# Performance work log

Measured on AMD Instinct MI355X. Metric: run time of the kernel, lower is better.

## Reference

```python
import jax, jax.numpy as jnp
import numpy as np

TEMPERATURE = 0.07


def setup_inputs() -> dict:
    key = jax.random.key(0)
    k1, k2 = jax.random.split(key)
    B, D = 8192, 256
    embeddings = jax.random.normal(k1, (B, D), dtype=jnp.float32)
    ids = jax.random.randint(k2, (B,), 0, 1024, dtype=jnp.int64 if jax.config.jax_enable_x64 else jnp.int32)
    return {"embeddings": embeddings, "ids": ids}


def reference(embeddings, ids):
    B = embeddings.shape[0]
    # L2-normalize rows (F.normalize with p=2, dim=1)
    emb = embeddings / jnp.maximum(jnp.linalg.norm(embeddings, axis=1, keepdims=True), 1e-12)
    sim = (emb @ emb.T) / TEMPERATURE                      # [B, B]
    eye = jnp.eye(B, dtype=bool)
    sim = jnp.where(eye, -jnp.inf, sim)
    exp_sim = jnp.exp(sim)                                  # diag -> 0
    pos_mask = (ids[:, None] == ids[None, :]) & ~eye        # [B, B]
    pos_sum = jnp.sum(jnp.where(pos_mask, exp_sim, 0.0), axis=1)  # [B]
    all_sum = jnp.sum(exp_sim, axis=1)                      # [B]
    valid = pos_mask.any(axis=1)
    per_row = -jnp.log(pos_sum / all_sum)
    loss = jnp.sum(jnp.where(valid, per_row, 0.0))
    n_valid = jnp.sum(valid.astype(jnp.float32))
    return loss / jnp.maximum(n_valid, 1.0)
```

## Files before the change

kernel.cpp:

```cpp
#include <hip/hip_runtime.h>
#include <hip/hip_bf16.h>

#define B_SZ 8192
#define D_SZ 256
#define NTILES 2080
#define GRID_SIM 512
#define PRESCALE 4.539816004686735f

typedef __attribute__((ext_vector_type(4))) float f32x4;
typedef __attribute__((ext_vector_type(8))) short s16x8;

__global__ __launch_bounds__(256) void norm_kernel(const float* __restrict__ emb,
                                                   ushort* __restrict__ nbf,
                                                   float* __restrict__ sums) {
    sums[blockIdx.x * 64 + (threadIdx.x >> 2)] = 0.0f;

    const int wave = threadIdx.x >> 6, lane = threadIdx.x & 63;
    for (int g = blockIdx.x; g < B_SZ / 4; g += 256) {
        const int row = g * 4 + wave;
        const float4 v = ((const float4*)(emb + (size_t)row * D_SZ))[lane];
        float ss = v.x * v.x + v.y * v.y + v.z * v.z + v.w * v.w;
        #pragma unroll
        for (int m = 1; m < 64; m <<= 1) ss += __shfl_xor(ss, m, 64);
        float s = PRESCALE / fmaxf(sqrtf(ss), 1e-12f);
        __hip_bfloat16 b0 = __float2bfloat16(v.x * s);
        __hip_bfloat16 b1 = __float2bfloat16(v.y * s);
        __hip_bfloat16 b2 = __float2bfloat16(v.z * s);
        __hip_bfloat16 b3 = __float2bfloat16(v.w * s);
        ushort4 o;
        o.x = *(ushort*)&b0; o.y = *(ushort*)&b1; o.z = *(ushort*)&b2; o.w = *(ushort*)&b3;
        ((ushort4*)(nbf + (size_t)row * D_SZ))[lane] = o;
    }
}

__device__ __forceinline__ void decode_tile(int tb, int& i0, int& j0, bool& diag) {
    int bj = (int)((sqrtf(8.0f * tb + 1.0f) - 1.0f) * 0.5f);
    while ((bj + 1) * (bj + 2) / 2 <= tb) ++bj;
    while (bj * (bj + 1) / 2 > tb) --bj;
    const int bi = tb - bj * (bj + 1) / 2;
    i0 = bi * 128; j0 = bj * 128; diag = (bi == bj);
}

__device__ __forceinline__ void gload16(const ushort* g, ushort* l) {
    __builtin_amdgcn_global_load_lds(
        (const __attribute__((address_space(1))) unsigned int*)g,
        (__attribute__((address_space(3))) unsigned int*)l,
        16, 0, 0);
}

__device__ __forceinline__ void issue_stage(ushort* bA,
                                            const ushort* __restrict__ N,
                                            int i0, int j0, int k0,
                                            int wave, int r, int c8s) {
    ushort* bB = bA + 8192;
    const ushort* gA = N + (size_t)(i0 + wave * 32) * D_SZ + k0;
    const ushort* gB = N + (size_t)(j0 + wave * 32) * D_SZ + k0;
    #pragma unroll
    for (int q = 0; q < 4; ++q) {
        gload16(gA + (size_t)(q * 8 + r) * D_SZ + c8s, bA + (wave * 32 + q * 8) * 64);
        gload16(gB + (size_t)(q * 8 + r) * D_SZ + c8s, bB + (wave * 32 + q * 8) * 64);
    }
}

__global__ __launch_bounds__(256) void sim_kernel(const ushort* __restrict__ N,
                                                  const int* __restrict__ ids,
                                                  float* __restrict__ all_sum,
                                                  float* __restrict__ pos_sum) {
    __shared__ ushort smem[4 * 128 * 64];

    const int t    = threadIdx.x;
    const int wave = t >> 6, lane = t & 63;
    const int wy   = wave >> 1, wx = wave & 1;
    const int r    = lane >> 3;
    const int c8s  = ((lane & 7) ^ r) * 8;
    const int myc  = lane & 15;

    int tb = blockIdx.x;
    int i0, j0; bool diag;
    decode_tile(tb, i0, j0, diag);

    issue_stage(smem, N, i0, j0, 0, wave, r, c8s);

    while (true) {
        const int ntb = tb + GRID_SIM;
        const bool have_next = (ntb < NTILES);
        int ni0 = i0, nj0 = j0; bool ndiag = diag;
        if (have_next) decode_tile(ntb, ni0, nj0, ndiag);

        f32x4 acc[4][4];
        #pragma unroll
        for (int mi = 0; mi < 4; ++mi)
            #pragma unroll
            for (int ni = 0; ni < 4; ++ni)
                acc[mi][ni] = (f32x4){0.f, 0.f, 0.f, 0.f};

        #pragma unroll
        for (int kk = 0; kk < 4; ++kk) {
            ushort* bA = smem + (kk & 1) * 16384;
            ushort* bW = smem + ((kk + 1) & 1) * 16384;
            ushort* bB = bA + 8192;

            asm volatile("s_waitcnt vmcnt(0)" ::: "memory");
            __syncthreads();
            if (kk < 3)           issue_stage(bW, N, i0, j0, (kk + 1) * 64, wave, r, c8s);
            else if (have_next)   issue_stage(bW, N, ni0, nj0, 0, wave, r, c8s);

            #pragma unroll
            for (int ks = 0; ks < 2; ++ks) {
                const int C = ks * 4 + (lane >> 4);
                const int slot = (C ^ (lane & 7)) * 8;
                s16x8 af[4], bf[4];
                #pragma unroll
                for (int mi = 0; mi < 4; ++mi)
                    af[mi] = *(const s16x8*)&bA[(wy * 64 + mi * 16 + (lane & 15)) * 64 + slot];
                #pragma unroll
                for (int ni = 0; ni < 4; ++ni)
                    bf[ni] = *(const s16x8*)&bB[(wx * 64 + ni * 16 + (lane & 15)) * 64 + slot];
                #pragma unroll
                for (int mi = 0; mi < 4; ++mi)
                    #pragma unroll
                    for (int ni = 0; ni < 4; ++ni)
                        acc[mi][ni] = __builtin_amdgcn_mfma_f32_16x16x32_bf16(
                            af[mi], bf[ni], acc[mi][ni], 0, 0, 0);
            }
        }

        __syncthreads();
        float* rowAllPart = (float*)&smem[16384];
        float* rowPosPart = (float*)&smem[24576];

        int idc[4];
        #pragma unroll
        for (int ni = 0; ni < 4; ++ni)
            idc[ni] = ids[j0 + wx * 64 + ni * 16 + myc];

        float cAll[4] = {0.f, 0.f, 0.f, 0.f};
        float cPos[4] = {0.f, 0.f, 0.f, 0.f};

        #pragma unroll
        for (int mi = 0; mi < 4; ++mi) {
            float rAll[4] = {0.f, 0.f, 0.f, 0.f};
            float rPos[4] = {0.f, 0.f, 0.f, 0.f};
            const int rbase = wy * 64 + mi * 16 + (lane >> 4) * 4;
            const int4 idr  = *(const int4*)&ids[i0 + rbase];
            #pragma unroll
            for (int ni = 0; ni < 4; ++ni) {
                const int cloc = wx * 64 + ni * 16 + myc;
                #pragma unroll
                for (int rg = 0; rg < 4; ++rg) {
                    const int lr = rbase + rg;
                    float e = __builtin_amdgcn_exp2f(acc[mi][ni][rg]);
                    if (diag && lr == cloc) e = 0.0f;
                    rAll[rg] += e; cAll[ni] += e;
                    const int idrv = (rg == 0) ? idr.x : (rg == 1) ? idr.y
                                   : (rg == 2) ? idr.z : idr.w;
                    if (idrv == idc[ni]) { rPos[rg] += e; cPos[ni] += e; }
                }
            }
            #pragma unroll
            for (int rg = 0; rg < 4; ++rg) {
                rowAllPart[(rbase + rg) * 32 + wx * 16 + myc] = rAll[rg];
                rowPosPart[(rbase + rg) * 32 + wx * 16 + myc] = rPos[rg];
            }
        }

        if (!diag) {
            #pragma unroll
            for (int ni = 0; ni < 4; ++ni) {
                cAll[ni] += __shfl_xor(cAll[ni], 16, 64);
                cAll[ni] += __shfl_xor(cAll[ni], 32, 64);
                cPos[ni] += __shfl_xor(cPos[ni], 16, 64);
                cPos[ni] += __shfl_xor(cPos[ni], 32, 64);
            }
            if (lane < 16) {
                #pragma unroll
                for (int ni = 0; ni < 4; ++ni) {
                    const int gc = j0 + wx * 64 + ni * 16 + lane;
                    atomicAdd(&all_sum[gc], cAll[ni]);
                    if (cPos[ni] != 0.0f) atomicAdd(&pos_sum[gc], cPos[ni]);
                }
            }
        }

        __syncthreads();
        {
            const int row = t & 127;
            const float* src = (t >= 128) ? rowPosPart : rowAllPart;
            float s = 0.0f;
            #pragma unroll
            for (int k8 = 0; k8 < 8; ++k8) {
                const int chunk = (k8 + (row & 7)) & 7;
                const float4 v = *(const float4*)&src[row * 32 + chunk * 4];
                s += v.x + v.y + v.z + v.w;
            }
            float* dst = (t >= 128) ? pos_sum : all_sum;
            atomicAdd(&dst[i0 + row], s);
        }

        if (!have_next) break;
        tb = ntb; i0 = ni0; j0 = nj0; diag = ndiag;
    }
}

__global__ __launch_bounds__(256) void loss_kernel(const float* __restrict__ all_sum,
                                                   const float* __restrict__ pos_sum,
                                                   float* __restrict__ out) {
    float loss = 0.0f, cnt = 0.0f;
    for (int i = threadIdx.x; i < B_SZ; i += 256) {
        float p = pos_sum[i], a = all_sum[i];
        if (p > 0.0f) { loss += logf(a) - logf(p); cnt += 1.0f; }
    }
    #pragma unroll
    for (int m = 1; m < 64; m <<= 1) {
        loss += __shfl_xor(loss, m, 64);
        cnt  += __shfl_xor(cnt, m, 64);
    }
    __shared__ float sl[4], sc[4];
    int wave = threadIdx.x >> 6, lane = threadIdx.x & 63;
    if (lane == 0) { sl[wave] = loss; sc[wave] = cnt; }
    __syncthreads();
    if (threadIdx.x == 0) {
        float L = sl[0] + sl[1] + sl[2] + sl[3];
        float C = sc[0] + sc[1] + sc[2] + sc[3];
        out[0] = L / fmaxf(C, 1.0f);
    }
}

extern "C" void kernel_launch(void* const* d_in, const int* in_sizes, int n_in,
                              void* d_out, int out_size, void* d_ws, size_t ws_size,
                              hipStream_t stream) {
    const float* emb = (const float*)d_in[0];
    const int*   ids = (const int*)d_in[1];
    float*       out = (float*)d_out;

    float*  all_sum = (float*)d_ws;
    float*  pos_sum = all_sum + B_SZ;
    ushort* nbf     = (ushort*)((char*)d_ws + 65536);

    norm_kernel<<<256, 256, 0, stream>>>(emb, nbf, all_sum);
    sim_kernel<<<GRID_SIM, 256, 0, stream>>>(nbf, ids, all_sum, pos_sum);
    loss_kernel<<<1, 256, 0, stream>>>(all_sum, pos_sum, out);
}
```

Before: 118.2 us.

## Use eight waves per tile and reduce row partials with shuffles

The similarity kernel now runs 512 threads per block (eight waves in a 2x4 grid), so each wave computes a 64x32 sub-tile instead of 64x64. Each wave loads half as many rows per stage, and register use per thread drops. Row partial sums are now reduced within the wave by xor shuffles and written to small dedicated shared arrays. This removes the 32-way shared-memory partial reduction and the extra barrier before the epilogue. More waves per CU should improve latency hiding, at the cost of more shuffle work and more LDS fragment reads per MFMA, since A fragments are reloaded by four waves instead of two.

```diff
diff --git a/kernel.cpp b/kernel.cpp
--- a/kernel.cpp
+++ b/kernel.cpp
@@ -53,27 +53,29 @@
                                             int i0, int j0, int k0,
                                             int wave, int r, int c8s) {
     ushort* bB = bA + 8192;
-    const ushort* gA = N + (size_t)(i0 + wave * 32) * D_SZ + k0;
-    const ushort* gB = N + (size_t)(j0 + wave * 32) * D_SZ + k0;
+    const ushort* gA = N + (size_t)(i0 + wave * 16) * D_SZ + k0;
+    const ushort* gB = N + (size_t)(j0 + wave * 16) * D_SZ + k0;
     #pragma unroll
-    for (int q = 0; q < 4; ++q) {
-        gload16(gA + (size_t)(q * 8 + r) * D_SZ + c8s, bA + (wave * 32 + q * 8) * 64);
-        gload16(gB + (size_t)(q * 8 + r) * D_SZ + c8s, bB + (wave * 32 + q * 8) * 64);
-    }
-}
-
-__global__ __launch_bounds__(256) void sim_kernel(const ushort* __restrict__ N,
-                                                  const int* __restrict__ ids,
-                                                  float* __restrict__ all_sum,
-                                                  float* __restrict__ pos_sum) {
+    for (int q = 0; q < 2; ++q) {
+        gload16(gA + (size_t)(q * 8 + r) * D_SZ + c8s, bA + (wave * 16 + q * 8) * 64);
+        gload16(gB + (size_t)(q * 8 + r) * D_SZ + c8s, bB + (wave * 16 + q * 8) * 64);
+    }
+}
+
+__global__ __launch_bounds__(512, 4) void sim_kernel(const ushort* __restrict__ N,
+                                                     const int* __restrict__ ids,
+                                                     float* __restrict__ all_sum,
+                                                     float* __restrict__ pos_sum) {
     __shared__ ushort smem[4 * 128 * 64];
+    __shared__ float rowAllPart[128 * 4];
+    __shared__ float rowPosPart[128 * 4];
 
     const int t    = threadIdx.x;
     const int wave = t >> 6, lane = t & 63;
-    const int wy   = wave >> 1, wx = wave & 1;
+    const int wy   = wave >> 2, wx = wave & 3;
     const int r    = lane >> 3;
     const int c8s  = ((lane & 7) ^ r) * 8;
-    const int myc  = lane & 15;
+    const int hi   = lane >> 4, myc = lane & 15;
 
     int tb = blockIdx.x;
     int i0, j0; bool diag;
@@ -87,11 +89,11 @@
         int ni0 = i0, nj0 = j0; bool ndiag = diag;
         if (have_next) decode_tile(ntb, ni0, nj0, ndiag);
 
-        f32x4 acc[4][4];
+        f32x4 acc[4][2];
         #pragma unroll
         for (int mi = 0; mi < 4; ++mi)
             #pragma unroll
-            for (int ni = 0; ni < 4; ++ni)
+            for (int ni = 0; ni < 2; ++ni)
                 acc[mi][ni] = (f32x4){0.f, 0.f, 0.f, 0.f};
 
         #pragma unroll
@@ -109,48 +111,43 @@
             for (int ks = 0; ks < 2; ++ks) {
                 const int C = ks * 4 + (lane >> 4);
                 const int slot = (C ^ (lane & 7)) * 8;
-                s16x8 af[4], bf[4];
+                s16x8 af[4], bf[2];
                 #pragma unroll
                 for (int mi = 0; mi < 4; ++mi)
                     af[mi] = *(const s16x8*)&bA[(wy * 64 + mi * 16 + (lane & 15)) * 64 + slot];
                 #pragma unroll
-                for (int ni = 0; ni < 4; ++ni)
-                    bf[ni] = *(const s16x8*)&bB[(wx * 64 + ni * 16 + (lane & 15)) * 64 + slot];
+                for (int ni = 0; ni < 2; ++ni)
+                    bf[ni] = *(const s16x8*)&bB[(wx * 32 + ni * 16 + (lane & 15)) * 64 + slot];
                 #pragma unroll
                 for (int mi = 0; mi < 4; ++mi)
                     #pragma unroll
-                    for (int ni = 0; ni < 4; ++ni)
+                    for (int ni = 0; ni < 2; ++ni)
                         acc[mi][ni] = __builtin_amdgcn_mfma_f32_16x16x32_bf16(
                             af[mi], bf[ni], acc[mi][ni], 0, 0, 0);
             }
         }
 
-        __syncthreads();
-        float* rowAllPart = (float*)&smem[16384];
-        float* rowPosPart = (float*)&smem[24576];
-
-        int idc[4];
-        #pragma unroll
-        for (int ni = 0; ni < 4; ++ni)
-            idc[ni] = ids[j0 + wx * 64 + ni * 16 + myc];
-
-        float cAll[4] = {0.f, 0.f, 0.f, 0.f};
-        float cPos[4] = {0.f, 0.f, 0.f, 0.f};
+        int idc[2];
+        #pragma unroll
+        for (int ni = 0; ni < 2; ++ni)
+            idc[ni] = ids[j0 + wx * 32 + ni * 16 + myc];
+
+        float cAll[2] = {0.f, 0.f};
+        float cPos[2] = {0.f, 0.f};
 
         #pragma unroll
         for (int mi = 0; mi < 4; ++mi) {
             float rAll[4] = {0.f, 0.f, 0.f, 0.f};
             float rPos[4] = {0.f, 0.f, 0.f, 0.f};
-            const int rbase = wy * 64 + mi * 16 + (lane >> 4) * 4;
+            const int rbase = wy * 64 + mi * 16 + hi * 4;
             const int4 idr  = *(const int4*)&ids[i0 + rbase];
             #pragma unroll
-            for (int ni = 0; ni < 4; ++ni) {
-                const int cloc = wx * 64 + ni * 16 + myc;
+            for (int ni = 0; ni < 2; ++ni) {
+                const int cloc = wx * 32 + ni * 16 + myc;
                 #pragma unroll
                 for (int rg = 0; rg < 4; ++rg) {
-                    const int lr = rbase + rg;
                     float e = __builtin_amdgcn_exp2f(acc[mi][ni][rg]);
-                    if (diag && lr == cloc) e = 0.0f;
+                    if (diag && (rbase + rg) == cloc) e = 0.0f;
                     rAll[rg] += e; cAll[ni] += e;
                     const int idrv = (rg == 0) ? idr.x : (rg == 1) ? idr.y
                                    : (rg == 2) ? idr.z : idr.w;
@@ -159,23 +156,33 @@
             }
             #pragma unroll
             for (int rg = 0; rg < 4; ++rg) {
-                rowAllPart[(rbase + rg) * 32 + wx * 16 + myc] = rAll[rg];
-                rowPosPart[(rbase + rg) * 32 + wx * 16 + myc] = rPos[rg];
+                #pragma unroll
+                for (int m = 1; m < 16; m <<= 1) {
+                    rAll[rg] += __shfl_xor(rAll[rg], m, 64);
+                    rPos[rg] += __shfl_xor(rPos[rg], m, 64);
+                }
+            }
+            if (myc == 0) {
+                #pragma unroll
+                for (int rg = 0; rg < 4; ++rg) {
+                    rowAllPart[(rbase + rg) * 4 + wx] = rAll[rg];
+                    rowPosPart[(rbase + rg) * 4 + wx] = rPos[rg];
+                }
             }
         }
 
         if (!diag) {
             #pragma unroll
-            for (int ni = 0; ni < 4; ++ni) {
+            for (int ni = 0; ni < 2; ++ni) {
                 cAll[ni] += __shfl_xor(cAll[ni], 16, 64);
                 cAll[ni] += __shfl_xor(cAll[ni], 32, 64);
                 cPos[ni] += __shfl_xor(cPos[ni], 16, 64);
                 cPos[ni] += __shfl_xor(cPos[ni], 32, 64);
             }
-            if (lane < 16) {
-                #pragma unroll
-                for (int ni = 0; ni < 4; ++ni) {
-                    const int gc = j0 + wx * 64 + ni * 16 + lane;
+            if (hi == 0) {
+                #pragma unroll
+                for (int ni = 0; ni < 2; ++ni) {
+                    const int gc = j0 + wx * 32 + ni * 16 + myc;
                     atomicAdd(&all_sum[gc], cAll[ni]);
                     if (cPos[ni] != 0.0f) atomicAdd(&pos_sum[gc], cPos[ni]);
                 }
@@ -183,16 +190,11 @@
         }
 
         __syncthreads();
-        {
+        if (t < 256) {
             const int row = t & 127;
-            const float* src = (t >= 128) ? rowPosPart : rowAllPart;
-            float s = 0.0f;
-            #pragma unroll
-            for (int k8 = 0; k8 < 8; ++k8) {
-                const int chunk = (k8 + (row & 7)) & 7;
-                const float4 v = *(const float4*)&src[row * 32 + chunk * 4];
-                s += v.x + v.y + v.z + v.w;
-            }
+            const float4 v = (t >= 128) ? *(const float4*)&rowPosPart[row * 4]
+                                        : *(const float4*)&rowAllPart[row * 4];
+            const float s = v.x + v.y + v.z + v.w;
             float* dst = (t >= 128) ? pos_sum : all_sum;
             atomicAdd(&dst[i0 + row], s);
         }
@@ -238,6 +240,6 @@
     ushort* nbf     = (ushort*)((char*)d_ws + 65536);
 
     norm_kernel<<<256, 256, 0, stream>>>(emb, nbf, all_sum);
-    sim_kernel<<<GRID_SIM, 256, 0, stream>>>(nbf, ids, all_sum, pos_sum);
+    sim_kernel<<<GRID_SIM, 512, 0, stream>>>(nbf, ids, all_sum, pos_sum);
     loss_kernel<<<1, 256, 0, stream>>>(all_sum, pos_sum, out);
 }
```

Measured after the change: 134.7 us. 14.0% more time.
